# Performance work log

Hardware: AMD Instinct MI355X
Metric: run time of the kernel (lower is better)

## Reference

```python
import jax, jax.numpy as jnp
import numpy as np

EPS = 1e-5

def layer_norm(x, w, b):
    m = jnp.mean(x, axis=-1, keepdims=True)
    v = jnp.mean(jnp.square(x - m), axis=-1, keepdims=True)
    return (x - m) * jax.lax.rsqrt(v + EPS) * w + b

def setup_inputs() -> dict:
    key = jax.random.key(0)
    B, S, D, H = 4, 2048, 768, 12
    Dh, F = D // H, 4 * D
    ks = jax.random.split(key, 16)
    s = 0.02
    return {
        "x":    jax.random.normal(ks[0], (B, S, D), dtype=jnp.float32),
        # per-head q/k/v projections stacked over heads: [H, D, Dh]
        "Wq":   jax.random.normal(ks[1], (H, D, Dh), dtype=jnp.float32) * s,
        "bq":   jnp.zeros((H, Dh), dtype=jnp.float32),
        "Wk":   jax.random.normal(ks[2], (H, D, Dh), dtype=jnp.float32) * s,
        "bk":   jnp.zeros((H, Dh), dtype=jnp.float32),
        "Wv":   jax.random.normal(ks[3], (H, D, Dh), dtype=jnp.float32) * s,
        "bv":   jnp.zeros((H, Dh), dtype=jnp.float32),
        "Wo":   jax.random.normal(ks[4], (D, D), dtype=jnp.float32) * s,
        "bo":   jnp.zeros((D,), dtype=jnp.float32),
        "W1":   jax.random.normal(ks[5], (D, F), dtype=jnp.float32) * s,
        "b1":   jnp.zeros((F,), dtype=jnp.float32),
        "W2":   jax.random.normal(ks[6], (F, D), dtype=jnp.float32) * s,
        "b2":   jnp.zeros((D,), dtype=jnp.float32),
        "ln1_w": jnp.ones((D,), dtype=jnp.float32),
        "ln1_b": jnp.zeros((D,), dtype=jnp.float32),
        "ln2_w": jnp.ones((D,), dtype=jnp.float32),
        "ln2_b": jnp.zeros((D,), dtype=jnp.float32),
    }

def reference(x, Wq, bq, Wk, bk, Wv, bv, Wo, bo, W1, b1, W2, b2,
              ln1_w, ln1_b, ln2_w, ln2_b):
    B, S, D = x.shape
    H, _, Dh = Wq.shape
    scale = jnp.sqrt(jnp.float32(Dh))  # torch scales by sqrt(dout)
    # q,k,v: [B, H, S, Dh]
    q = jnp.einsum('bsd,hde->bhse', x, Wq) + bq[None, :, None, :]
    k = jnp.einsum('bsd,hde->bhse', x, Wk) + bk[None, :, None, :]
    v = jnp.einsum('bsd,hde->bhse', x, Wv) + bv[None, :, None, :]
    scores = jnp.einsum('bhqe,bhke->bhqk', q, k) / scale  # [B,H,S,S]
    causal = jnp.tril(jnp.ones((S, S), dtype=bool))
    scores = jnp.where(causal[None, None], scores, -jnp.inf)
    attn = jax.nn.softmax(scores, axis=-1)
    ctx = jnp.einsum('bhqk,bhke->bhqe', attn, v)           # [B,H,S,Dh]
    ctx = jnp.transpose(ctx, (0, 2, 1, 3)).reshape(B, S, D)  # concat heads
    att_out = ctx @ Wo + bo
    h = layer_norm(x + att_out, ln1_w, ln1_b)  # post-norm, dropout=0
    ff = jax.nn.gelu(h @ W1 + b1, approximate=False) @ W2 + b2
    return layer_norm(h + ff, ln2_w, ln2_b)
```

## Files before the change

kernel.cpp:

```cpp
#include <hip/hip_runtime.h>
#include <hip/hip_bf16.h>
#include <math.h>

#define B_ 4
#define S_ 2048
#define D_ 768
#define H_ 12
#define DH_ 64
#define F_ 3072
#define NTOK (B_*S_)
#define BH_ (B_*H_)

typedef __hip_bfloat16 bf16;
typedef __attribute__((ext_vector_type(8))) short bf16x8;
typedef __attribute__((ext_vector_type(4))) float f32x4;
typedef __attribute__((ext_vector_type(4))) _Float16 half4;
typedef __attribute__((ext_vector_type(8))) _Float16 half8;

#define GLD16(g, l) __builtin_amdgcn_global_load_lds( \
    (__attribute__((address_space(1))) void*)(uintptr_t)(g), \
    (__attribute__((address_space(3))) void*)(uintptr_t)(l), 16, 0, 0)

__device__ __forceinline__ float bs2f(short s){
  union { unsigned int u; float f; } cv; cv.u = ((unsigned int)(unsigned short)s) << 16; return cv.f;
}
__device__ __forceinline__ float b2f(bf16 v){ return __bfloat162float(v); }
__device__ __forceinline__ bf16 f2b(float v){ return __float2bfloat16(v); }
__device__ __forceinline__ short f2bb(float v){ bf16 b = f2b(v); short s; __builtin_memcpy(&s, &b, 2); return s; }

__device__ __forceinline__ void wgbar(){
  __builtin_amdgcn_s_barrier();
  asm volatile("" ::: "memory");
}

__device__ __forceinline__ float gelu_fast(float v){
  const float c0 = -2.302208157f;
  const float c1 = -0.102943238f;
  float w = v*v;
  float z = v * __builtin_fmaf(c1, w, c0);
  float t = __builtin_amdgcn_exp2f(z);
  return v * __builtin_amdgcn_rcpf(1.0f + t);
}

__global__ void f32_to_bf16_k(const float* __restrict__ in, bf16* __restrict__ out, int n){
  int i = blockIdx.x*256 + threadIdx.x;
  if (i < n) out[i] = f2b(in[i]);
}

__global__ __launch_bounds__(256) void transpose_f32_bf16_k(const float* __restrict__ in,
    bf16* __restrict__ out, int K, int N){
  __shared__ float t[32][33];
  const int kb = blockIdx.y*32, nb = blockIdx.x*32;
  const int x = threadIdx.x & 31, y = threadIdx.x >> 5;
#pragma unroll
  for (int yy = y; yy < 32; yy += 8)
    t[yy][x] = in[(size_t)(kb+yy)*N + nb + x];
  __syncthreads();
#pragma unroll
  for (int yy = y; yy < 32; yy += 8)
    out[(size_t)(nb+yy)*K + kb + x] = f2b(t[x][yy]);
}

__global__ void pack_qkv_t_k(const float* __restrict__ Wq, const float* __restrict__ bq,
                             const float* __restrict__ Wk, const float* __restrict__ bk,
                             const float* __restrict__ Wv, const float* __restrict__ bv,
                             bf16* __restrict__ Wt, float* __restrict__ bcat){
  int idx = blockIdx.x*256 + threadIdx.x;
  if (idx < 3*D_*D_){
    int n = idx / D_;
    int k = idx - n*D_;
    int which = n / D_;
    int cc = n - which*D_;
    int h = cc >> 6, e = cc & 63;
    const float* W = (which==0) ? Wq : ((which==1) ? Wk : Wv);
    Wt[idx] = f2b(W[((size_t)h*D_ + k)*DH_ + e]);
  }
  if (idx < 3*D_){
    int which = idx / D_;
    int cc = idx - which*D_;
    int h = cc >> 6, e = cc & 63;
    const float* bb = (which==0) ? bq : ((which==1) ? bk : bv);
    bcat[idx] = bb[h*DH_ + e];
  }
}

#define STAGE_A(bufi_, kh_, kt_) do { \
    GLD16(gA  + (size_t)(kt_)*64 + (kh_)*32, asb + ((bufi_)<<15) + ((kh_)<<14)); \
    GLD16(gA2 + (size_t)(kt_)*64 + (kh_)*32, asb + ((bufi_)<<15) + ((kh_)<<14) + 8192); } while(0)
#define STAGE_B(bufi_, kh_, kt_) do { \
    GLD16(gB  + (size_t)(kt_)*64 + (kh_)*32, bsb + ((bufi_)<<15) + ((kh_)<<14)); \
    GLD16(gB2 + (size_t)(kt_)*64 + (kh_)*32, bsb + ((bufi_)<<15) + ((kh_)<<14) + 8192); } while(0)
#define AFRAG(bufi_, ks_, i_) (*(const bf16x8*)(AsB + ((bufi_)<<15) + ((ks_)<<14) + ((wm + (i_)*16 + l16)<<6) + fsw))
#define BFRAG(bufi_, ks_, j_) (*(const bf16x8*)(BsB + ((bufi_)<<15) + ((ks_)<<14) + ((wn + (j_)*16 + l16)<<6) + fsw))

template<int EPI>
__global__ __launch_bounds__(512, 2) void mgemm256_k(
    const bf16* __restrict__ A, const bf16* __restrict__ Bt,
    const float* __restrict__ bias, bf16* __restrict__ C,
    int M, int N, int K,
    bf16* __restrict__ qb, bf16* __restrict__ kbuf, _Float16* __restrict__ vt)
{
  __shared__ __align__(16) bf16 As[32768];
  __shared__ __align__(16) bf16 Bs[32768];
  const int tid  = threadIdx.x;
  const int wave = tid >> 6, lane = tid & 63;
  const int quad = lane >> 4, l16 = lane & 15;
  const int wm = (wave >> 2) * 128;
  const int wn = (wave & 3) * 64;

  const int NX = gridDim.x;
  const int f  = blockIdx.y * NX + blockIdx.x;
  const int xcd = f & 7;
  const int j0  = f >> 3;
  const int bx  = j0 % NX;
  const int by  = (j0 / NX) * 8 + xcd;
  const int m0 = by * 256, n0 = bx * 256;

  const int srow = tid >> 2;
  const int sg   = (tid & 3) ^ ((tid >> 3) & 3);
  const bf16* gA  = A  + (size_t)(m0 + srow)*K + sg*8;
  const bf16* gA2 = A  + (size_t)(m0 + 128 + srow)*K + sg*8;
  const bf16* gB  = Bt + (size_t)(n0 + srow)*K + sg*8;
  const bf16* gB2 = Bt + (size_t)(n0 + 128 + srow)*K + sg*8;
  const uintptr_t asb = (uintptr_t)(void*)As + (size_t)wave*1024;
  const uintptr_t bsb = (uintptr_t)(void*)Bs + (size_t)wave*1024;

  const char* AsB = (const char*)As;
  const char* BsB = (const char*)Bs;
  const int fsw = (quad ^ ((l16 >> 1) & 3)) * 16;

  f32x4 acc[8][4];
#pragma unroll
  for (int i=0;i<8;i++)
#pragma unroll
    for (int j2=0;j2<4;j2++) acc[i][j2] = (f32x4)0.f;

  const int KT = K >> 6;

  STAGE_A(0, 0, 0); STAGE_B(0, 0, 0); STAGE_A(0, 1, 0); STAGE_B(0, 1, 0);
  asm volatile("s_waitcnt vmcnt(4)" ::: "memory");
  wgbar();

  for (int kt = 0; kt < KT; ++kt){
    const int bufc = kt & 1, bufn = bufc ^ 1;
    const bool pf = (kt + 1) < KT;
    bf16x8 af[4], bfr[4];

#pragma unroll
    for (int i=0;i<4;i++) af[i] = AFRAG(bufc, 0, i);
#pragma unroll
    for (int j2=0;j2<4;j2++) bfr[j2] = BFRAG(bufc, 0, j2);
    if (pf) STAGE_A(bufn, 0, kt+1);
    wgbar();
    __builtin_amdgcn_s_setprio(1);
#pragma unroll
    for (int i=0;i<4;i++)
#pragma unroll
      for (int j2=0;j2<4;j2++)
        acc[i][j2] = __builtin_amdgcn_mfma_f32_16x16x32_bf16(af[i], bfr[j2], acc[i][j2], 0, 0, 0);
    __builtin_amdgcn_s_setprio(0);
    wgbar();

#pragma unroll
    for (int i=0;i<4;i++) af[i] = AFRAG(bufc, 0, 4+i);
    if (pf) STAGE_B(bufn, 0, kt+1);
    wgbar();
    __builtin_amdgcn_s_setprio(1);
#pragma unroll
    for (int i=0;i<4;i++)
#pragma unroll
      for (int j2=0;j2<4;j2++)
        acc[4+i][j2] = __builtin_amdgcn_mfma_f32_16x16x32_bf16(af[i], bfr[j2], acc[4+i][j2], 0, 0, 0);
    __builtin_amdgcn_s_setprio(0);
    if (pf) asm volatile("s_waitcnt vmcnt(4)" ::: "memory");
    else    asm volatile("s_waitcnt vmcnt(0)" ::: "memory");
    wgbar();

#pragma unroll
    for (int i=0;i<4;i++) af[i] = AFRAG(bufc, 1, i);
#pragma unroll
    for (int j2=0;j2<4;j2++) bfr[j2] = BFRAG(bufc, 1, j2);
    if (pf) STAGE_A(bufn, 1, kt+1);
    wgbar();
    __builtin_amdgcn_s_setprio(1);
#pragma unroll
    for (int i=0;i<4;i++)
#pragma unroll
      for (int j2=0;j2<4;j2++)
        acc[i][j2] = __builtin_amdgcn_mfma_f32_16x16x32_bf16(af[i], bfr[j2], acc[i][j2], 0, 0, 0);
    __builtin_amdgcn_s_setprio(0);
    wgbar();

#pragma unroll
    for (int i=0;i<4;i++) af[i] = AFRAG(bufc, 1, 4+i);
    if (pf) STAGE_B(bufn, 1, kt+1);
    wgbar();
    __builtin_amdgcn_s_setprio(1);
#pragma unroll
    for (int i=0;i<4;i++)
#pragma unroll
      for (int j2=0;j2<4;j2++)
        acc[4+i][j2] = __builtin_amdgcn_mfma_f32_16x16x32_bf16(af[i], bfr[j2], acc[4+i][j2], 0, 0, 0);
    __builtin_amdgcn_s_setprio(0);
    if (pf) asm volatile("s_waitcnt vmcnt(4)" ::: "memory");
    wgbar();
  }

#pragma unroll
  for (int i=0;i<8;i++){
#pragma unroll
    for (int j2=0;j2<4;j2++){
      const int n = n0 + wn + j2*16 + l16;
      const int m_base = m0 + wm + i*16 + quad*4;
      if (EPI == 0){
        const int which = n / D_;
        const int cc = n - which*D_;
        const int h = cc >> 6, e = cc & 63;
        if (which == 2){
          const int b = m_base >> 11, s = m_base & (S_-1);
          const int sl = s & 63;
          const int perm = ((sl>>2)&3)*16 + ((sl>>4)&3)*4;
          half4 hv;
#pragma unroll
          for (int r=0;r<4;r++) hv[r] = (_Float16)(acc[i][j2][r] + bias[n]);
          *(half4*)(vt + ((size_t)(b*H_+h)*DH_ + e)*S_ + (s & ~63) + perm) = hv;
        } else {
          bf16* dst = (which==0) ? qb : kbuf;
          const float sc2 = (which==0) ? 0.125f : 1.0f;
#pragma unroll
          for (int r=0;r<4;r++){
            const int m = m_base + r;
            const int b = m >> 11, s = m & (S_-1);
            dst[((size_t)(b*H_+h)*S_ + s)*DH_ + e] = f2b((acc[i][j2][r] + bias[n]) * sc2);
          }
        }
      } else {
#pragma unroll
        for (int r=0;r<4;r++){
          const int m = m_base + r;
          float v = acc[i][j2][r] + bias[n];
          C[(size_t)m*N + n] = f2b(gelu_fast(v));
        }
      }
    }
  }
}
#undef STAGE_A
#undef STAGE_B
#undef AFRAG
#undef BFRAG

__global__ __launch_bounds__(256) void mgemm64_k(
    const bf16* __restrict__ A, const bf16* __restrict__ Bt,
    const float* __restrict__ bias, const bf16* __restrict__ aux,
    bf16* __restrict__ C, int M, int N, int K)
{
  __shared__ bf16 As[4096];
  __shared__ bf16 Bs[8192];
  const int tid  = threadIdx.x;
  const int wave = tid >> 6, lane = tid & 63;
  const int quad = lane >> 4, l16 = lane & 15;
  const int wm = (wave >> 1) * 32, wn = (wave & 1) * 64;

  const int NX = gridDim.x;
  const int f  = blockIdx.y * NX + blockIdx.x;
  const int xcd = f & 7;
  const int j   = f >> 3;
  const int bx  = j % NX;
  const int by  = (j / NX) * 8 + xcd;
  const int m0 = by * 64, n0 = bx * 128;

  const int srow8 = lane >> 3;
  const int g     = (lane & 7) ^ srow8;
  const bf16* gA0 = A  + (size_t)(m0 + wave*16 +      srow8)*K + g*8;
  const bf16* gA1 = A  + (size_t)(m0 + wave*16 +  8 + srow8)*K + g*8;
  const bf16* gB0 = Bt + (size_t)(n0 + wave*32 +      srow8)*K + g*8;
  const bf16* gB1 = Bt + (size_t)(n0 + wave*32 +  8 + srow8)*K + g*8;
  const bf16* gB2 = Bt + (size_t)(n0 + wave*32 + 16 + srow8)*K + g*8;
  const bf16* gB3 = Bt + (size_t)(n0 + wave*32 + 24 + srow8)*K + g*8;
  const uintptr_t asb = (uintptr_t)(void*)As + (size_t)wave*16*128;
  const uintptr_t bsb = (uintptr_t)(void*)Bs + (size_t)wave*32*128;

  f32x4 acc[2][4];
#pragma unroll
  for (int i=0;i<2;i++)
#pragma unroll
    for (int j2=0;j2<4;j2++) acc[i][j2] = (f32x4)0.f;

  const char* AsB = (const char*)As;
  const char* BsB = (const char*)Bs;

  for (int k0 = 0; k0 < K; k0 += 64){
    __syncthreads();
    GLD16(gA0, asb);
    GLD16(gA1, asb + 1024);
    GLD16(gB0, bsb);
    GLD16(gB1, bsb + 1024);
    GLD16(gB2, bsb + 2048);
    GLD16(gB3, bsb + 3072);
    gA0 += 64; gA1 += 64; gB0 += 64; gB1 += 64; gB2 += 64; gB3 += 64;
    __syncthreads();
#pragma unroll
    for (int kq = 0; kq < 2; kq++){
      const int cbase = kq*4 + quad;
      bf16x8 af[2], bfr[4];
#pragma unroll
      for (int i=0;i<2;i++){
        const int m = wm + i*16 + l16;
        af[i] = *(const bf16x8*)(AsB + (m << 7) + ((cbase ^ (m & 7)) << 4));
      }
#pragma unroll
      for (int j2=0;j2<4;j2++){
        const int n = wn + j2*16 + l16;
        bfr[j2] = *(const bf16x8*)(BsB + (n << 7) + ((cbase ^ (n & 7)) << 4));
      }
#pragma unroll
      for (int i=0;i<2;i++)
#pragma unroll
        for (int j2=0;j2<4;j2++)
          acc[i][j2] = __builtin_amdgcn_mfma_f32_16x16x32_bf16(af[i], bfr[j2], acc[i][j2], 0, 0, 0);
    }
  }

#pragma unroll
  for (int i=0;i<2;i++){
#pragma unroll
    for (int j2=0;j2<4;j2++){
      const int n = n0 + wn + j2*16 + l16;
      const int m_base = m0 + wm + i*16 + quad*4;
#pragma unroll
      for (int r=0;r<4;r++){
        const int m = m_base + r;
        float v = acc[i][j2][r] + bias[n] + b2f(aux[(size_t)m*N + n]);
        C[(size_t)m*N + n] = f2b(v);
      }
    }
  }
}

__global__ __launch_bounds__(256) void fattn_k(const bf16* __restrict__ qb,
    const bf16* __restrict__ kb, const _Float16* __restrict__ vt, bf16* __restrict__ ctx)
{
  __shared__ __align__(16) char smem[19456];
  bf16     (*Ks)[72] = (bf16(*)[72])smem;
  _Float16 (*Vs)[72] = (_Float16(*)[72])(smem + 9216);
  float* maxb  = (float*)(smem + 18432);
  float* libuf = (float*)(smem + 18944);
  float* Obuf  = (float*)smem;

  const int bh = blockIdx.x;
  const int qt = 31 - blockIdx.y;
  const int q0 = qt * 64;
  const int tid = threadIdx.x;
  const int wave = tid >> 6, lane = tid & 63;
  const int quad = lane >> 4, l16 = lane & 15;
  const int kh = wave >> 1, qh = wave & 1;
  const size_t kbase = (size_t)bh * S_ * DH_;

  bf16x8 qf[2][2];
#pragma unroll
  for (int nf=0; nf<2; nf++)
#pragma unroll
    for (int h=0; h<2; h++)
      qf[nf][h] = *(const bf16x8*)(qb + kbase + (size_t)(q0 + qh*32 + nf*16 + l16)*DH_ + h*32 + quad*8);

  f32x4 o[4][2];
#pragma unroll
  for (int df=0; df<4; df++){ o[df][0] = (f32x4)0.f; o[df][1] = (f32x4)0.f; }
  float mi[2] = {-1e30f, -1e30f}, li[2] = {0.f, 0.f};

  for (int kt = 0; kt <= qt; ++kt){
    const int k0 = kt * 64;
    __syncthreads();
    {
      const int r = tid >> 2, seg = (tid & 3) * 16;
      const bf16* ksrc = kb + kbase + (size_t)(k0 + r)*DH_ + seg;
      bf16x8 ka = *(const bf16x8*)ksrc;
      bf16x8 kc2 = *(const bf16x8*)(ksrc + 8);
      *(bf16x8*)&Ks[r][seg]   = ka;
      *(bf16x8*)&Ks[r][seg+8] = kc2;
      const _Float16* vsrc = vt + ((size_t)bh*DH_ + r)*S_ + k0 + seg;
      half8 va = *(const half8*)vsrc;
      half8 vb2 = *(const half8*)(vsrc + 8);
      *(half8*)&Vs[r][seg]   = va;
      *(half8*)&Vs[r][seg+8] = vb2;
    }
    __syncthreads();

    bf16x8 af[2][2];
#pragma unroll
    for (int mf=0; mf<2; mf++)
#pragma unroll
      for (int h=0; h<2; h++)
        af[mf][h] = *(const bf16x8*)&Ks[kh*32 + mf*16 + l16][h*32 + quad*8];
    f32x4 sc[2][2];
#pragma unroll
    for (int mf=0; mf<2; mf++)
#pragma unroll
      for (int nf=0; nf<2; nf++){
        f32x4 t = __builtin_amdgcn_mfma_f32_16x16x32_bf16(af[mf][0], qf[nf][0], (f32x4)0.f, 0, 0, 0);
        sc[mf][nf] = __builtin_amdgcn_mfma_f32_16x16x32_bf16(af[mf][1], qf[nf][1], t, 0, 0, 0);
      }

    if (kt == qt){
#pragma unroll
      for (int mf=0; mf<2; mf++){
        const int keyl = kh*32 + mf*16 + quad*4;
#pragma unroll
        for (int nf=0; nf<2; nf++){
          const int ql = qh*32 + nf*16 + l16;
#pragma unroll
          for (int r=0; r<4; r++)
            if (keyl + r > ql) sc[mf][nf][r] = -1e30f;
        }
      }
    }

    float mw[2];
#pragma unroll
    for (int nf=0; nf<2; nf++){
      float mx = -1e30f;
#pragma unroll
      for (int mf=0; mf<2; mf++)
#pragma unroll
        for (int r=0; r<4; r++) mx = fmaxf(mx, sc[mf][nf][r]);
      mx = fmaxf(mx, __shfl_xor(mx, 16));
      mx = fmaxf(mx, __shfl_xor(mx, 32));
      mw[nf] = mx;
    }
    if (quad == 0){
      maxb[kh*64 + qh*32 + l16]      = mw[0];
      maxb[kh*64 + qh*32 + 16 + l16] = mw[1];
    }
    __syncthreads();

    half4 pf[2][2];
    float alpha[2];
#pragma unroll
    for (int nf=0; nf<2; nf++){
      const float mo = maxb[(1-kh)*64 + qh*32 + nf*16 + l16];
      const float mn = fmaxf(mi[nf], fmaxf(mw[nf], mo));
      alpha[nf] = __expf(mi[nf] - mn);
      mi[nf] = mn;
      float rs = 0.f;
#pragma unroll
      for (int mf=0; mf<2; mf++)
#pragma unroll
        for (int r=0; r<4; r++){
          float p = __expf(sc[mf][nf][r] - mn);
          pf[mf][nf][r] = (_Float16)p;
          rs += p;
        }
      rs += __shfl_xor(rs, 16);
      rs += __shfl_xor(rs, 32);
      li[nf] = li[nf]*alpha[nf] + rs;
    }

#pragma unroll
    for (int df=0; df<4; df++)
#pragma unroll
      for (int nf=0; nf<2; nf++)
#pragma unroll
        for (int r=0; r<4; r++) o[df][nf][r] *= alpha[nf];

#pragma unroll
    for (int df=0; df<4; df++){
      half8 vv = *(const half8*)&Vs[df*16 + l16][quad*16 + kh*8];
      half4 vlo = __builtin_shufflevector(vv, vv, 0,1,2,3);
      half4 vhi = __builtin_shufflevector(vv, vv, 4,5,6,7);
#pragma unroll
      for (int nf=0; nf<2; nf++){
        o[df][nf] = __builtin_amdgcn_mfma_f32_16x16x16f16(vlo, pf[0][nf], o[df][nf], 0, 0, 0);
        o[df][nf] = __builtin_amdgcn_mfma_f32_16x16x16f16(vhi, pf[1][nf], o[df][nf], 0, 0, 0);
      }
    }
  }

  __syncthreads();
  if (quad == 0){
    libuf[kh*64 + qh*32 + l16]      = li[0];
    libuf[kh*64 + qh*32 + 16 + l16] = li[1];
  }
  if (kh == 1){
#pragma unroll
    for (int df=0; df<4; df++)
#pragma unroll
      for (int nf=0; nf<2; nf++)
#pragma unroll
        for (int r=0; r<4; r++)
          Obuf[(qh*64 + df*16 + quad*4 + r)*33 + nf*16 + l16] = o[df][nf][r];
  }
  __syncthreads();
  if (kh == 0){
    const int b = bh / H_, h = bh - (bh / H_)*H_;
#pragma unroll
    for (int nf=0; nf<2; nf++){
      const int q64 = qh*32 + nf*16 + l16;
      const float inv = 1.0f / (libuf[q64] + libuf[64 + q64]);
      const int qtok = q0 + q64;
#pragma unroll
      for (int df=0; df<4; df++){
        short4 pk;
        float v0 = (o[df][nf][0] + Obuf[(qh*64 + df*16 + quad*4 + 0)*33 + nf*16 + l16]) * inv;
        float v1 = (o[df][nf][1] + Obuf[(qh*64 + df*16 + quad*4 + 1)*33 + nf*16 + l16]) * inv;
        float v2 = (o[df][nf][2] + Obuf[(qh*64 + df*16 + quad*4 + 2)*33 + nf*16 + l16]) * inv;
        float v3 = (o[df][nf][3] + Obuf[(qh*64 + df*16 + quad*4 + 3)*33 + nf*16 + l16]) * inv;
        pk.x = f2bb(v0); pk.y = f2bb(v1); pk.z = f2bb(v2); pk.w = f2bb(v3);
        *(short4*)((short*)ctx + ((size_t)(b*S_ + qtok))*D_ + h*DH_ + df*16 + quad*4) = pk;
      }
    }
  }
}

template<typename T> __device__ __forceinline__ void stf(T* p, float v);
template<> __device__ __forceinline__ void stf<float>(float* p, float v){ *p = v; }
template<> __device__ __forceinline__ void stf<bf16>(bf16* p, float v){ *p = f2b(v); }

template<typename OutT>
__global__ __launch_bounds__(256) void layernorm_k(const bf16* __restrict__ X,
    const float* __restrict__ g, const float* __restrict__ bta, OutT* __restrict__ Y)
{
  const int row = blockIdx.x;
  const int tid = threadIdx.x;
  const bf16* xr = X + (size_t)row * D_;
  float vals[3];
  float s = 0.f, s2 = 0.f;
#pragma unroll
  for (int i = 0; i < 3; i++){
    float v = b2f(xr[tid + i*256]);
    vals[i] = v; s += v; s2 += v*v;
  }
#pragma unroll
  for (int o = 32; o > 0; o >>= 1){ s += __shfl_down(s, o); s2 += __shfl_down(s2, o); }
  __shared__ float rs[4], rq[4];
  const int lane = tid & 63, w = tid >> 6;
  if (lane == 0){ rs[w] = s; rq[w] = s2; }
  __syncthreads();
  s  = rs[0]+rs[1]+rs[2]+rs[3];
  s2 = rq[0]+rq[1]+rq[2]+rq[3];
  const float mean = s * (1.0f/D_);
  const float var  = s2 * (1.0f/D_) - mean*mean;
  const float inv  = rsqrtf(var + 1e-5f);
#pragma unroll
  for (int i = 0; i < 3; i++){
    int c = tid + i*256;
    float o = (vals[i] - mean) * inv * g[c] + bta[c];
    stf(Y + (size_t)row*D_ + c, o);
  }
}

extern "C" void kernel_launch(void* const* d_in, const int* in_sizes, int n_in,
                              void* d_out, int out_size, void* d_ws, size_t ws_size,
                              hipStream_t stream)
{
  const float* x   = (const float*)d_in[0];
  const float* Wq  = (const float*)d_in[1];
  const float* bq  = (const float*)d_in[2];
  const float* Wk  = (const float*)d_in[3];
  const float* bk  = (const float*)d_in[4];
  const float* Wv  = (const float*)d_in[5];
  const float* bv  = (const float*)d_in[6];
  const float* Wo  = (const float*)d_in[7];
  const float* bo  = (const float*)d_in[8];
  const float* W1  = (const float*)d_in[9];
  const float* b1  = (const float*)d_in[10];
  const float* W2  = (const float*)d_in[11];
  const float* b2  = (const float*)d_in[12];
  const float* g1  = (const float*)d_in[13];
  const float* be1 = (const float*)d_in[14];
  const float* g2  = (const float*)d_in[15];
  const float* be2 = (const float*)d_in[16];
  float* out = (float*)d_out;

  char* ws = (char*)d_ws;
  size_t off = 0;
  auto alloc = [&](size_t bytes)->char*{
    char* p = ws + off; off = (off + bytes + 255) & ~(size_t)255; return p;
  };
  bf16*  xb    = (bf16*) alloc((size_t)NTOK*D_*2);
  bf16*  WcatT = (bf16*) alloc((size_t)3*D_*D_*2);
  float* bcat  = (float*)alloc((size_t)3*D_*4);
  bf16*  WoT   = (bf16*) alloc((size_t)D_*D_*2);
  bf16*  W1T   = (bf16*) alloc((size_t)F_*D_*2);
  bf16*  W2T   = (bf16*) alloc((size_t)D_*F_*2);
  bf16*  r1    = (bf16*) alloc((size_t)NTOK*F_*2);
  bf16*  qb    = r1;
  bf16*  kb    = r1 + (size_t)NTOK*D_;
  _Float16* vt = (_Float16*)(r1 + (size_t)2*NTOK*D_);
  bf16*  ff1   = r1;
  bf16*  ctxb  = (bf16*) alloc((size_t)NTOK*D_*2);
  bf16*  y1    = (bf16*) alloc((size_t)NTOK*D_*2);
  bf16*  hb    = (bf16*) alloc((size_t)NTOK*D_*2);
  bf16*  y2    = ctxb;

  f32_to_bf16_k<<<(NTOK*D_+255)/256, 256, 0, stream>>>(x, xb, NTOK*D_);
  transpose_f32_bf16_k<<<dim3(D_/32, D_/32), 256, 0, stream>>>(Wo, WoT, D_, D_);
  transpose_f32_bf16_k<<<dim3(F_/32, D_/32), 256, 0, stream>>>(W1, W1T, D_, F_);
  transpose_f32_bf16_k<<<dim3(D_/32, F_/32), 256, 0, stream>>>(W2, W2T, F_, D_);
  pack_qkv_t_k<<<(3*D_*D_+255)/256, 256, 0, stream>>>(Wq,bq,Wk,bk,Wv,bv,WcatT,bcat);

  mgemm256_k<0><<<dim3(3*D_/256, NTOK/256), 512, 0, stream>>>(
      xb, WcatT, bcat, nullptr, NTOK, 3*D_, D_, qb, kb, vt);

  fattn_k<<<dim3(BH_, S_/64), 256, 0, stream>>>(qb, kb, vt, ctxb);

  mgemm64_k<<<dim3(D_/128, NTOK/64), 256, 0, stream>>>(
      ctxb, WoT, bo, xb, y1, NTOK, D_, D_);

  layernorm_k<bf16><<<NTOK, 256, 0, stream>>>(y1, g1, be1, hb);

  mgemm256_k<2><<<dim3(F_/256, NTOK/256), 512, 0, stream>>>(
      hb, W1T, b1, ff1, NTOK, F_, D_, nullptr, nullptr, nullptr);

  mgemm64_k<<<dim3(D_/128, NTOK/64), 256, 0, stream>>>(
      ff1, W2T, b2, hb, y2, NTOK, D_, F_);

  layernorm_k<float><<<NTOK, 256, 0, stream>>>(y2, g2, be2, out);
}
```

Measured before the change: 410.3 us.

## Double-buffer mgemm64, lazy softmax rescale in attention, vectorize conversion and layernorm

Several independent changes land together. mgemm64 now double-buffers its LDS tiles, prefetching the next K tile while MFMAs run on the current one. The attention softmax moves to base-2 exponentials by folding log2(e) into the Q scale, and it skips the accumulator rescale unless the running max grows by more than 8. The f32-to-bf16 conversion and layernorm kernels use 4-wide vector loads and stores, with layernorm at 192 threads per row. The lazy rescale relies on a bounded fp16 P range and changes how the max is written back for merging, which adds some numerical risk.

```diff
diff --git a/kernel.cpp b/kernel.cpp
--- a/kernel.cpp
+++ b/kernel.cpp
@@ -42,9 +42,14 @@
   return v * __builtin_amdgcn_rcpf(1.0f + t);
 }
 
-__global__ void f32_to_bf16_k(const float* __restrict__ in, bf16* __restrict__ out, int n){
+__global__ void f32_to_bf16_k(const float4* __restrict__ in, short4* __restrict__ out, int n4){
   int i = blockIdx.x*256 + threadIdx.x;
-  if (i < n) out[i] = f2b(in[i]);
+  if (i < n4){
+    float4 v = in[i];
+    short4 o;
+    o.x = f2bb(v.x); o.y = f2bb(v.y); o.z = f2bb(v.z); o.w = f2bb(v.w);
+    out[i] = o;
+  }
 }
 
 __global__ __launch_bounds__(256) void transpose_f32_bf16_k(const float* __restrict__ in,
@@ -226,7 +231,7 @@
           *(half4*)(vt + ((size_t)(b*H_+h)*DH_ + e)*S_ + (s & ~63) + perm) = hv;
         } else {
           bf16* dst = (which==0) ? qb : kbuf;
-          const float sc2 = (which==0) ? 0.125f : 1.0f;
+          const float sc2 = (which==0) ? 0.18033688f : 1.0f;
 #pragma unroll
           for (int r=0;r<4;r++){
             const int m = m_base + r;
@@ -255,8 +260,8 @@
     const float* __restrict__ bias, const bf16* __restrict__ aux,
     bf16* __restrict__ C, int M, int N, int K)
 {
-  __shared__ bf16 As[4096];
-  __shared__ bf16 Bs[8192];
+  __shared__ bf16 As[8192];
+  __shared__ bf16 Bs[16384];
   const int tid  = threadIdx.x;
   const int wave = tid >> 6, lane = tid & 63;
   const int quad = lane >> 4, l16 = lane & 15;
@@ -289,17 +294,34 @@
 
   const char* AsB = (const char*)As;
   const char* BsB = (const char*)Bs;
-
-  for (int k0 = 0; k0 < K; k0 += 64){
-    __syncthreads();
-    GLD16(gA0, asb);
-    GLD16(gA1, asb + 1024);
-    GLD16(gB0, bsb);
-    GLD16(gB1, bsb + 1024);
-    GLD16(gB2, bsb + 2048);
-    GLD16(gB3, bsb + 3072);
-    gA0 += 64; gA1 += 64; gB0 += 64; gB1 += 64; gB2 += 64; gB3 += 64;
-    __syncthreads();
+  const int KT = K >> 6;
+
+  GLD16(gA0, asb);
+  GLD16(gA1, asb + 1024);
+  GLD16(gB0, bsb);
+  GLD16(gB1, bsb + 1024);
+  GLD16(gB2, bsb + 2048);
+  GLD16(gB3, bsb + 3072);
+  gA0 += 64; gA1 += 64; gB0 += 64; gB1 += 64; gB2 += 64; gB3 += 64;
+  asm volatile("s_waitcnt vmcnt(0)" ::: "memory");
+  wgbar();
+
+  for (int kt = 0; kt < KT; ++kt){
+    const int cur = kt & 1, nxt = cur ^ 1;
+    const bool pf = (kt + 1) < KT;
+    if (pf){
+      const uintptr_t ao = asb + nxt*8192;
+      const uintptr_t bo = bsb + nxt*16384;
+      GLD16(gA0, ao);
+      GLD16(gA1, ao + 1024);
+      GLD16(gB0, bo);
+      GLD16(gB1, bo + 1024);
+      GLD16(gB2, bo + 2048);
+      GLD16(gB3, bo + 3072);
+      gA0 += 64; gA1 += 64; gB0 += 64; gB1 += 64; gB2 += 64; gB3 += 64;
+    }
+    const char* Ac = AsB + cur*8192;
+    const char* Bc = BsB + cur*16384;
 #pragma unroll
     for (int kq = 0; kq < 2; kq++){
       const int cbase = kq*4 + quad;
@@ -307,12 +329,12 @@
 #pragma unroll
       for (int i=0;i<2;i++){
         const int m = wm + i*16 + l16;
-        af[i] = *(const bf16x8*)(AsB + (m << 7) + ((cbase ^ (m & 7)) << 4));
+        af[i] = *(const bf16x8*)(Ac + (m << 7) + ((cbase ^ (m & 7)) << 4));
       }
 #pragma unroll
       for (int j2=0;j2<4;j2++){
         const int n = wn + j2*16 + l16;
-        bfr[j2] = *(const bf16x8*)(BsB + (n << 7) + ((cbase ^ (n & 7)) << 4));
+        bfr[j2] = *(const bf16x8*)(Bc + (n << 7) + ((cbase ^ (n & 7)) << 4));
       }
 #pragma unroll
       for (int i=0;i<2;i++)
@@ -320,6 +342,8 @@
         for (int j2=0;j2<4;j2++)
           acc[i][j2] = __builtin_amdgcn_mfma_f32_16x16x32_bf16(af[i], bfr[j2], acc[i][j2], 0, 0, 0);
     }
+    if (pf) asm volatile("s_waitcnt vmcnt(0)" ::: "memory");
+    wgbar();
   }
 
 #pragma unroll
@@ -434,34 +458,38 @@
     }
     __syncthreads();
 
+    const float tm0 = fmaxf(mw[0], maxb[(1-kh)*64 + qh*32 + l16]);
+    const float tm1 = fmaxf(mw[1], maxb[(1-kh)*64 + qh*32 + 16 + l16]);
+    const bool need = !__all((tm0 - mi[0] <= 8.f) && (tm1 - mi[1] <= 8.f));
+    if (need){
+      const float mn0 = fmaxf(mi[0], tm0);
+      const float mn1 = fmaxf(mi[1], tm1);
+      const float a0 = __builtin_amdgcn_exp2f(mi[0] - mn0);
+      const float a1 = __builtin_amdgcn_exp2f(mi[1] - mn1);
+      mi[0] = mn0; mi[1] = mn1;
+      li[0] *= a0; li[1] *= a1;
+#pragma unroll
+      for (int df=0; df<4; df++)
+#pragma unroll
+        for (int r=0; r<4; r++){ o[df][0][r] *= a0; o[df][1][r] *= a1; }
+    }
+
     half4 pf[2][2];
-    float alpha[2];
 #pragma unroll
     for (int nf=0; nf<2; nf++){
-      const float mo = maxb[(1-kh)*64 + qh*32 + nf*16 + l16];
-      const float mn = fmaxf(mi[nf], fmaxf(mw[nf], mo));
-      alpha[nf] = __expf(mi[nf] - mn);
-      mi[nf] = mn;
       float rs = 0.f;
 #pragma unroll
       for (int mf=0; mf<2; mf++)
 #pragma unroll
         for (int r=0; r<4; r++){
-          float p = __expf(sc[mf][nf][r] - mn);
+          float p = __builtin_amdgcn_exp2f(sc[mf][nf][r] - mi[nf]);
           pf[mf][nf][r] = (_Float16)p;
           rs += p;
         }
       rs += __shfl_xor(rs, 16);
       rs += __shfl_xor(rs, 32);
-      li[nf] = li[nf]*alpha[nf] + rs;
-    }
-
-#pragma unroll
-    for (int df=0; df<4; df++)
-#pragma unroll
-      for (int nf=0; nf<2; nf++)
-#pragma unroll
-        for (int r=0; r<4; r++) o[df][nf][r] *= alpha[nf];
+      li[nf] += rs;
+    }
 
 #pragma unroll
     for (int df=0; df<4; df++){
@@ -480,6 +508,10 @@
   if (quad == 0){
     libuf[kh*64 + qh*32 + l16]      = li[0];
     libuf[kh*64 + qh*32 + 16 + l16] = li[1];
+  }
+  if (quad == 1){
+    maxb[kh*64 + qh*32 + l16]      = mi[0];
+    maxb[kh*64 + qh*32 + 16 + l16] = mi[1];
   }
   if (kh == 1){
 #pragma unroll
@@ -512,41 +544,42 @@
   }
 }
 
-template<typename T> __device__ __forceinline__ void stf(T* p, float v);
-template<> __device__ __forceinline__ void stf<float>(float* p, float v){ *p = v; }
-template<> __device__ __forceinline__ void stf<bf16>(bf16* p, float v){ *p = f2b(v); }
+template<typename T> __device__ __forceinline__ void st4(T* p, size_t idx, float a, float b, float c, float d);
+template<> __device__ __forceinline__ void st4<float>(float* p, size_t idx, float a, float b, float c, float d){
+  float4 v; v.x=a; v.y=b; v.z=c; v.w=d; *(float4*)(p+idx) = v;
+}
+template<> __device__ __forceinline__ void st4<bf16>(bf16* p, size_t idx, float a, float b, float c, float d){
+  short4 v; v.x=f2bb(a); v.y=f2bb(b); v.z=f2bb(c); v.w=f2bb(d); *(short4*)((short*)p+idx) = v;
+}
 
 template<typename OutT>
-__global__ __launch_bounds__(256) void layernorm_k(const bf16* __restrict__ X,
+__global__ __launch_bounds__(192) void layernorm_k(const bf16* __restrict__ X,
     const float* __restrict__ g, const float* __restrict__ bta, OutT* __restrict__ Y)
 {
   const int row = blockIdx.x;
   const int tid = threadIdx.x;
-  const bf16* xr = X + (size_t)row * D_;
-  float vals[3];
-  float s = 0.f, s2 = 0.f;
-#pragma unroll
-  for (int i = 0; i < 3; i++){
-    float v = b2f(xr[tid + i*256]);
-    vals[i] = v; s += v; s2 += v*v;
-  }
+  const short4 raw = *(const short4*)((const short*)X + (size_t)row*D_ + tid*4);
+  const float v0 = bs2f(raw.x), v1 = bs2f(raw.y), v2 = bs2f(raw.z), v3 = bs2f(raw.w);
+  float s  = v0+v1+v2+v3;
+  float s2 = v0*v0+v1*v1+v2*v2+v3*v3;
 #pragma unroll
   for (int o = 32; o > 0; o >>= 1){ s += __shfl_down(s, o); s2 += __shfl_down(s2, o); }
-  __shared__ float rs[4], rq[4];
+  __shared__ float rs[3], rq[3];
   const int lane = tid & 63, w = tid >> 6;
   if (lane == 0){ rs[w] = s; rq[w] = s2; }
   __syncthreads();
-  s  = rs[0]+rs[1]+rs[2]+rs[3];
-  s2 = rq[0]+rq[1]+rq[2]+rq[3];
+  s  = rs[0]+rs[1]+rs[2];
+  s2 = rq[0]+rq[1]+rq[2];
   const float mean = s * (1.0f/D_);
   const float var  = s2 * (1.0f/D_) - mean*mean;
   const float inv  = rsqrtf(var + 1e-5f);
-#pragma unroll
-  for (int i = 0; i < 3; i++){
-    int c = tid + i*256;
-    float o = (vals[i] - mean) * inv * g[c] + bta[c];
-    stf(Y + (size_t)row*D_ + c, o);
-  }
+  const float4 g4 = *(const float4*)(g + tid*4);
+  const float4 b4 = *(const float4*)(bta + tid*4);
+  st4(Y, (size_t)row*D_ + tid*4,
+      (v0-mean)*inv*g4.x + b4.x,
+      (v1-mean)*inv*g4.y + b4.y,
+      (v2-mean)*inv*g4.z + b4.z,
+      (v3-mean)*inv*g4.w + b4.w);
 }
 
 extern "C" void kernel_launch(void* const* d_in, const int* in_sizes, int n_in,
@@ -593,7 +626,8 @@
   bf16*  hb    = (bf16*) alloc((size_t)NTOK*D_*2);
   bf16*  y2    = ctxb;
 
-  f32_to_bf16_k<<<(NTOK*D_+255)/256, 256, 0, stream>>>(x, xb, NTOK*D_);
+  f32_to_bf16_k<<<(NTOK*D_/4+255)/256, 256, 0, stream>>>(
+      (const float4*)x, (short4*)xb, NTOK*D_/4);
   transpose_f32_bf16_k<<<dim3(D_/32, D_/32), 256, 0, stream>>>(Wo, WoT, D_, D_);
   transpose_f32_bf16_k<<<dim3(F_/32, D_/32), 256, 0, stream>>>(W1, W1T, D_, F_);
   transpose_f32_bf16_k<<<dim3(D_/32, F_/32), 256, 0, stream>>>(W2, W2T, F_, D_);
@@ -607,7 +641,7 @@
   mgemm64_k<<<dim3(D_/128, NTOK/64), 256, 0, stream>>>(
       ctxb, WoT, bo, xb, y1, NTOK, D_, D_);
 
-  layernorm_k<bf16><<<NTOK, 256, 0, stream>>>(y1, g1, be1, hb);
+  layernorm_k<bf16><<<NTOK, 192, 0, stream>>>(y1, g1, be1, hb);
 
   mgemm256_k<2><<<dim3(F_/256, NTOK/256), 512, 0, stream>>>(
       hb, W1T, b1, ff1, NTOK, F_, D_, nullptr, nullptr, nullptr);
@@ -615,5 +649,5 @@
   mgemm64_k<<<dim3(D_/128, NTOK/64), 256, 0, stream>>>(
       ff1, W2T, b2, hb, y2, NTOK, D_, F_);
 
-  layernorm_k<float><<<NTOK, 256, 0, stream>>>(y2, g2, be2, out);
-}
+  layernorm_k<float><<<NTOK, 192, 0, stream>>>(y2, g2, be2, out);
+}
```

Result: faster. 401.3 us (-2.2%).
